# Performance work log

Hardware: AMD Instinct MI355X
Metric: run time of the kernel (lower is better)

The kernel has to match this reference:

```python
import jax, jax.numpy as jnp
import numpy as np

N = 50000      # nodes
E = 800000     # edges
G = 2000       # graphs
F_IN = 34
HID = 256
H = 8
D = 32         # HID // H
L = 5


def _layer_norm(x, g, b, eps=1e-5):
    m = x.mean(-1, keepdims=True)
    v = ((x - m) ** 2).mean(-1, keepdims=True)
    return (x - m) / jnp.sqrt(v + eps) * g + b


def _gelu(x):
    return jax.nn.gelu(x, approximate=False)  # torch exact GELU


def _segment_softmax(scores, seg, n):
    # scores: [E', H], seg: [E'] target node ids
    m = jax.ops.segment_max(scores, seg, num_segments=n)
    m = jnp.where(jnp.isfinite(m), m, 0.0)
    ex = jnp.exp(scores - m[seg])
    den = jax.ops.segment_sum(ex, seg, num_segments=n)
    return ex / (den[seg] + 1e-16)


def setup_inputs() -> dict:
    key = jax.random.key(0)
    ks = iter(jax.random.split(key, 64))

    def p(shape, fan):
        return (jax.random.normal(next(ks), shape, jnp.float32) / np.sqrt(fan)).astype(jnp.float32)

    inp = {}
    inp['x'] = jax.random.normal(next(ks), (N, F_IN), jnp.float32)
    inp['edge_index'] = jax.random.randint(next(ks), (2, E), 0, N, jnp.int32)
    inp['batch'] = jnp.sort(jax.random.randint(next(ks), (N,), 0, G, jnp.int32))

    # input embed
    inp['in_W'] = p((F_IN, HID), F_IN); inp['in_b'] = jnp.zeros((HID,), jnp.float32)
    inp['in_ln_g'] = jnp.ones((HID,), jnp.float32); inp['in_ln_b'] = jnp.zeros((HID,), jnp.float32)
    # 5 GATv2 layers (stacked on leading dim)
    inp['gat_Wl'] = p((L, HID, HID), HID); inp['gat_bl'] = jnp.zeros((L, HID), jnp.float32)
    inp['gat_Wr'] = p((L, HID, HID), HID); inp['gat_br'] = jnp.zeros((L, HID), jnp.float32)
    inp['gat_att'] = p((L, H, D), D)
    inp['gat_bias'] = jnp.zeros((L, HID), jnp.float32)
    inp['gat_ln_g'] = jnp.ones((L, HID), jnp.float32); inp['gat_ln_b'] = jnp.zeros((L, HID), jnp.float32)
    # TransformerConv
    inp['tr_Wq'] = p((HID, HID), HID); inp['tr_bq'] = jnp.zeros((HID,), jnp.float32)
    inp['tr_Wk'] = p((HID, HID), HID); inp['tr_bk'] = jnp.zeros((HID,), jnp.float32)
    inp['tr_Wv'] = p((HID, HID), HID); inp['tr_bv'] = jnp.zeros((HID,), jnp.float32)
    inp['tr_Wskip'] = p((HID, HID), HID); inp['tr_bskip'] = jnp.zeros((HID,), jnp.float32)
    inp['tr_ln_g'] = jnp.ones((HID,), jnp.float32); inp['tr_ln_b'] = jnp.zeros((HID,), jnp.float32)
    # output proj
    inp['out_W'] = p((2 * HID, 2 * HID), 2 * HID); inp['out_b'] = jnp.zeros((2 * HID,), jnp.float32)
    inp['out_ln_g'] = jnp.ones((2 * HID,), jnp.float32); inp['out_ln_b'] = jnp.zeros((2 * HID,), jnp.float32)
    return inp


def reference(x, edge_index, batch,
              in_W, in_b, in_ln_g, in_ln_b,
              gat_Wl, gat_bl, gat_Wr, gat_br, gat_att, gat_bias, gat_ln_g, gat_ln_b,
              tr_Wq, tr_bq, tr_Wk, tr_bk, tr_Wv, tr_bv, tr_Wskip, tr_bskip, tr_ln_g, tr_ln_b,
              out_W, out_b, out_ln_g, out_ln_b):
    # input embedding (dropout inactive in eval)
    h = _gelu(_layer_norm(x @ in_W + in_b, in_ln_g, in_ln_b))

    src, dst = edge_index[0], edge_index[1]  # PyG: row=source j, col=target i
    loops = jnp.arange(N, dtype=src.dtype)
    s2 = jnp.concatenate([src, loops])  # GATv2 adds self loops
    d2 = jnp.concatenate([dst, loops])

    for l in range(L):  # small fixed loop over layers
        xl = (h @ gat_Wl[l] + gat_bl[l]).reshape(N, H, D)  # source transform / message
        xr = (h @ gat_Wr[l] + gat_br[l]).reshape(N, H, D)  # target transform
        e = jax.nn.leaky_relu(xl[s2] + xr[d2], 0.2)        # [E', H, D]
        score = jnp.einsum('ehd,hd->eh', e, gat_att[l])
        alpha = _segment_softmax(score, d2, N)             # softmax over incoming edges
        out = jax.ops.segment_sum(xl[s2] * alpha[..., None], d2, num_segments=N)
        out = out.reshape(N, HID) + gat_bias[l]
        h = h + _gelu(_layer_norm(out, gat_ln_g[l], gat_ln_b[l]))

    # TransformerConv (no self loops, root_weight skip connection)
    q = (h @ tr_Wq + tr_bq).reshape(N, H, D)
    k = (h @ tr_Wk + tr_bk).reshape(N, H, D)
    v = (h @ tr_Wv + tr_bv).reshape(N, H, D)
    score = (q[dst] * k[src]).sum(-1) / jnp.sqrt(jnp.float32(D))  # [E, H]
    alpha = _segment_softmax(score, dst, N)
    out = jax.ops.segment_sum(v[src] * alpha[..., None], dst, num_segments=N).reshape(N, HID)
    out = out + h @ tr_Wskip + tr_bskip
    h = h + _layer_norm(out, tr_ln_g, tr_ln_b)

    # global mean + max pool
    cnt = jax.ops.segment_sum(jnp.ones((N,), h.dtype), batch, num_segments=G)
    h_mean = jax.ops.segment_sum(h, batch, num_segments=G) / jnp.maximum(cnt, 1.0)[:, None]
    h_max = jax.ops.segment_max(h, batch, num_segments=G)
    h_max = jnp.where(jnp.isfinite(h_max), h_max, 0.0)
    ge = jnp.concatenate([h_mean, h_max], axis=-1)  # [G, 512]
    return _gelu(_layer_norm(ge @ out_W + out_b, out_ln_g, out_ln_b))
```

## Files before the change

kernel.cpp:

```cpp
#include <hip/hip_runtime.h>
#include <math.h>

#define N_NODES 50000
#define N_EDGES 800000
#define N_GRAPH 2000
#define F_INPUT 34
#define HID 256
#define NLAYER 5

typedef __attribute__((ext_vector_type(8))) short short8;
typedef __attribute__((ext_vector_type(4))) float float4v;

__device__ __forceinline__ float gelu_f(float x) {
  return 0.5f * x * (1.0f + erff(x * 0.70710678118654752440f));
}
__device__ __forceinline__ unsigned short bfr(float f) {
  unsigned u = __float_as_uint(f);
  return (unsigned short)((u + 0x7fffu + ((u >> 16) & 1u)) >> 16);
}
__device__ __forceinline__ float b2f(unsigned short s) {
  return __uint_as_float(((unsigned)s) << 16);
}
__device__ __forceinline__ float4 ld4bf(const unsigned short* p) {
  ushort4 u = *(const ushort4*)p;
  float4 f;
  f.x = b2f(u.x); f.y = b2f(u.y); f.z = b2f(u.z); f.w = b2f(u.w);
  return f;
}
__device__ __forceinline__ void acp16(const unsigned short* g, unsigned short* l) {
  __builtin_amdgcn_global_load_lds(
      (const __attribute__((address_space(1))) void*)g,
      (__attribute__((address_space(3))) void*)l, 16, 0, 0);
}

__global__ __launch_bounds__(256) void gemm_bias(
    const float* __restrict__ A, const float* __restrict__ B,
    const float* __restrict__ bias, float* __restrict__ C,
    int M, int Nn, int K) {
  __shared__ float As[16][64];
  __shared__ float Bs[16][64];
  int tid = threadIdx.x;
  int tx = tid & 15, ty = tid >> 4;
  int row0 = blockIdx.y * 64;
  int col0 = blockIdx.x * 64;
  float acc[4][4] = {};
  int a_r = tid >> 2;
  int a_c = (tid & 3) * 4;
  int b_r = tid >> 4;
  int b_c = (tid & 15) * 4;

  for (int k0 = 0; k0 < K; k0 += 16) {
    int ar = row0 + a_r;
#pragma unroll
    for (int i = 0; i < 4; ++i) {
      int kc = k0 + a_c + i;
      As[a_c + i][a_r] = (ar < M && kc < K) ? A[(long)ar * K + kc] : 0.f;
    }
    int bk = k0 + b_r;
    if (bk < K) {
      float4 bv = *(const float4*)&B[(long)bk * Nn + col0 + b_c];
      Bs[b_r][b_c + 0] = bv.x; Bs[b_r][b_c + 1] = bv.y;
      Bs[b_r][b_c + 2] = bv.z; Bs[b_r][b_c + 3] = bv.w;
    } else {
      Bs[b_r][b_c + 0] = 0.f; Bs[b_r][b_c + 1] = 0.f;
      Bs[b_r][b_c + 2] = 0.f; Bs[b_r][b_c + 3] = 0.f;
    }
    __syncthreads();
#pragma unroll
    for (int kk = 0; kk < 16; ++kk) {
      float4 a = *(const float4*)&As[kk][ty * 4];
      float4 b = *(const float4*)&Bs[kk][tx * 4];
      float av[4] = {a.x, a.y, a.z, a.w};
      float bv[4] = {b.x, b.y, b.z, b.w};
#pragma unroll
      for (int i = 0; i < 4; ++i)
#pragma unroll
        for (int j = 0; j < 4; ++j) acc[i][j] += av[i] * bv[j];
    }
    __syncthreads();
  }
  float4 bi = *(const float4*)&bias[col0 + tx * 4];
  float bia[4] = {bi.x, bi.y, bi.z, bi.w};
#pragma unroll
  for (int i = 0; i < 4; ++i) {
    int r = row0 + ty * 4 + i;
    if (r < M) {
      float4 o;
      o.x = acc[i][0] + bia[0]; o.y = acc[i][1] + bia[1];
      o.z = acc[i][2] + bia[2]; o.w = acc[i][3] + bia[3];
      *(float4*)&C[(long)r * Nn + col0 + tx * 4] = o;
    }
  }
}

__global__ __launch_bounds__(256) void gemm_mfma(
    const unsigned short* __restrict__ A, const unsigned short* __restrict__ Bt,
    const float* __restrict__ bias, void* __restrict__ Cv,
    int M, int Nn, int K, int flags) {
  __shared__ unsigned short smem[12288];
  unsigned short* As = smem;
  unsigned short* Bs = smem + 4096;
  int tid = threadIdx.x;
  int wave = tid >> 6, lane = tid & 63;
  int row0 = blockIdx.y * 128;
  int col0 = blockIdx.x * 128;
  int wm0 = (wave >> 1) * 64;
  int wn0 = (wave & 1) * 64;
  int q = lane >> 4;
  int ln = lane & 15;

  int srow = wave * 16 + (lane >> 2);
  int scol = (lane & 3) * 8;
  int ra0 = min(row0 + srow, M - 1);
  int ra1 = min(row0 + srow + 64, M - 1);
  const unsigned short* pa0 = A + (size_t)ra0 * K + scol;
  const unsigned short* pa1 = A + (size_t)ra1 * K + scol;
  const unsigned short* pb0 = Bt + (size_t)(col0 + srow) * K + scol;
  const unsigned short* pb1 = Bt + (size_t)(col0 + srow + 64) * K + scol;
  unsigned short* la0 = As + wave * 512;
  unsigned short* la1 = As + wave * 512 + 2048;
  unsigned short* lb0 = Bs + wave * 512;
  unsigned short* lb1 = Bs + wave * 512 + 2048;

  float4v acc[4][4];
#pragma unroll
  for (int i = 0; i < 4; ++i)
#pragma unroll
    for (int j = 0; j < 4; ++j) acc[i][j] = (float4v)0.f;

  for (int k0 = 0; k0 < K; k0 += 32) {
    acp16(pa0 + k0, la0);
    acp16(pa1 + k0, la1);
    acp16(pb0 + k0, lb0);
    acp16(pb1 + k0, lb1);
    __syncthreads();
    short8 af[4], bf[4];
#pragma unroll
    for (int i = 0; i < 4; ++i)
      af[i] = *(const short8*)&As[(wm0 + i * 16 + ln) * 32 + q * 8];
#pragma unroll
    for (int j = 0; j < 4; ++j)
      bf[j] = *(const short8*)&Bs[(wn0 + j * 16 + ln) * 32 + q * 8];
#pragma unroll
    for (int i = 0; i < 4; ++i)
#pragma unroll
      for (int j = 0; j < 4; ++j)
        acc[i][j] = __builtin_amdgcn_mfma_f32_16x16x32_bf16(af[i], bf[j], acc[i][j], 0, 0, 0);
    __syncthreads();
  }
  int rb = (lane >> 4) * 4;
  if (flags & 2) {
    unsigned short* Cb = (unsigned short*)Cv;
    unsigned short* eb = smem + wave * 2560;
#pragma unroll
    for (int p = 0; p < 2; ++p) {
#pragma unroll
      for (int jj = 0; jj < 2; ++jj) {
        int j = p * 2 + jj;
        float bv = bias[col0 + wn0 + j * 16 + ln];
#pragma unroll
        for (int i = 0; i < 4; ++i)
#pragma unroll
          for (int r = 0; r < 4; ++r)
            eb[(i * 16 + rb + r) * 40 + jj * 16 + ln] = bfr(acc[i][j][r] + bv);
      }
      int grow = row0 + wm0 + lane;
      uint4 w0 = *(uint4*)&eb[lane * 40 + 0];
      uint4 w1 = *(uint4*)&eb[lane * 40 + 8];
      uint4 w2 = *(uint4*)&eb[lane * 40 + 16];
      uint4 w3 = *(uint4*)&eb[lane * 40 + 24];
      if (grow < M) {
        unsigned short* dst = Cb + (size_t)grow * Nn + col0 + wn0 + p * 32;
        *(uint4*)&dst[0] = w0;
        *(uint4*)&dst[8] = w1;
        *(uint4*)&dst[16] = w2;
        *(uint4*)&dst[24] = w3;
      }
    }
  } else {
    float* C = (float*)Cv;
#pragma unroll
    for (int j = 0; j < 4; ++j) {
      int col = col0 + wn0 + j * 16 + ln;
      float bv = bias[col];
#pragma unroll
      for (int i = 0; i < 4; ++i)
#pragma unroll
        for (int r = 0; r < 4; ++r) {
          int row = row0 + wm0 + i * 16 + rb + r;
          if (row < M) C[(size_t)row * Nn + col] = acc[i][j][r] + bv;
        }
    }
  }
}

__global__ __launch_bounds__(256) void prep_w(
    const float* __restrict__ Wl, const float* __restrict__ Wr,
    const float* __restrict__ Wq, const float* __restrict__ Wk,
    const float* __restrict__ Wv, const float* __restrict__ Wsk,
    unsigned short* __restrict__ out) {
  __shared__ float t[32][33];
  int m = blockIdx.z;
  const float* W = (m < 10) ? (((m & 1) ? Wr : Wl) + (size_t)(m >> 1) * 65536)
                 : (m == 10) ? Wq : (m == 11) ? Wk : (m == 12) ? Wv : Wsk;
  int k0 = blockIdx.y * 32, n0 = blockIdx.x * 32;
  int r = threadIdx.x >> 5, c = threadIdx.x & 31;
  for (int rr = r; rr < 32; rr += 8)
    t[rr][c] = W[(size_t)(k0 + rr) * HID + n0 + c];
  __syncthreads();
  unsigned short* o = out + (size_t)m * 65536;
  for (int rr = r; rr < 32; rr += 8)
    o[(size_t)(n0 + rr) * HID + k0 + c] = bfr(t[c][rr]);
}

__global__ __launch_bounds__(256) void prep_wout(const float* __restrict__ W,
                                                 unsigned short* __restrict__ o) {
  __shared__ float t[32][33];
  int k0 = blockIdx.y * 32, n0 = blockIdx.x * 32;
  int r = threadIdx.x >> 5, c = threadIdx.x & 31;
  for (int rr = r; rr < 32; rr += 8)
    t[rr][c] = W[(size_t)(k0 + rr) * 512 + n0 + c];
  __syncthreads();
  for (int rr = r; rr < 32; rr += 8)
    o[(size_t)(n0 + rr) * 512 + k0 + c] = bfr(t[c][rr]);
}

__global__ __launch_bounds__(256) void prep_bias(
    const float* __restrict__ bl, const float* __restrict__ br,
    const float* __restrict__ bq, const float* __restrict__ bk,
    const float* __restrict__ bv, float* __restrict__ out) {
  int i = blockIdx.x * 256 + threadIdx.x;
  if (i < 2560) {
    int l = i >> 9, c = i & 511;
    out[i] = (c < 256) ? bl[l * 256 + c] : br[l * 256 + (c - 256)];
  } else if (i < 3328) {
    int j = i - 2560;
    out[i] = (j < 256) ? bq[j] : (j < 512) ? bk[j - 256] : bv[j - 512];
  }
}

__global__ __launch_bounds__(256) void ln_act(
    const float* __restrict__ in, const float* __restrict__ gam,
    const float* __restrict__ bet, float* __restrict__ out,
    unsigned short* __restrict__ outb,
    int n_rows, int width, int do_gelu) {
  int wid = blockIdx.x * 4 + (threadIdx.x >> 6);
  int lane = threadIdx.x & 63;
  if (wid >= n_rows) return;
  int chunks = width >> 8;
  float4 v[2];
  float s = 0.f;
  for (int c = 0; c < chunks; ++c) {
    int off = c * 256 + lane * 4;
    float4 t = *(const float4*)&in[(size_t)wid * width + off];
    v[c] = t;
    s += t.x + t.y + t.z + t.w;
  }
  for (int o = 1; o < 64; o <<= 1) s += __shfl_xor(s, o);
  float mean = s / (float)width;
  float vs = 0.f;
  for (int c = 0; c < chunks; ++c) {
    float dx = v[c].x - mean, dy = v[c].y - mean, dz = v[c].z - mean, dw = v[c].w - mean;
    vs += dx * dx + dy * dy + dz * dz + dw * dw;
  }
  for (int o = 1; o < 64; o <<= 1) vs += __shfl_xor(vs, o);
  float inv = rsqrtf(vs / (float)width + 1e-5f);
  for (int c = 0; c < chunks; ++c) {
    int off = c * 256 + lane * 4;
    float4 g4 = *(const float4*)&gam[off];
    float4 b4 = *(const float4*)&bet[off];
    float y[4] = {(v[c].x - mean) * inv * g4.x + b4.x,
                  (v[c].y - mean) * inv * g4.y + b4.y,
                  (v[c].z - mean) * inv * g4.z + b4.z,
                  (v[c].w - mean) * inv * g4.w + b4.w};
    if (do_gelu) {
#pragma unroll
      for (int i = 0; i < 4; ++i) y[i] = gelu_f(y[i]);
    }
    size_t idx = (size_t)wid * width + off;
    float4 o4 = {y[0], y[1], y[2], y[3]};
    *(float4*)&out[idx] = o4;
    if (outb) {
      ushort4 ob = {bfr(y[0]), bfr(y[1]), bfr(y[2]), bfr(y[3])};
      *(ushort4*)&outb[idx] = ob;
    }
  }
}

__global__ __launch_bounds__(256) void edge_count(const int* __restrict__ ei,
                                                  int* __restrict__ counts) {
  int e = blockIdx.x * 256 + threadIdx.x;
  if (e < N_EDGES) atomicAdd(&counts[ei[N_EDGES + e]], 1);
}

__global__ __launch_bounds__(1024) void scan1(const int* __restrict__ counts,
                                              int* __restrict__ indptr,
                                              int* __restrict__ bsums, int n) {
  __shared__ int sm[1024];
  int tid = threadIdx.x;
  int i = blockIdx.x * 1024 + tid;
  int v = (i < n) ? counts[i] : 0;
  sm[tid] = v;
  __syncthreads();
  for (int off = 1; off < 1024; off <<= 1) {
    int t = (tid >= off) ? sm[tid - off] : 0;
    __syncthreads();
    sm[tid] += t;
    __syncthreads();
  }
  if (i < n) indptr[i] = sm[tid] - v;
  if (tid == 1023) bsums[blockIdx.x] = sm[1023];
}

__global__ void scan2(int* __restrict__ bsums, int nb) {
  if (threadIdx.x == 0 && blockIdx.x == 0) {
    int acc = 0;
    for (int i = 0; i < nb; ++i) { int t = bsums[i]; bsums[i] = acc; acc += t; }
  }
}

__global__ __launch_bounds__(256) void scan3(const int* __restrict__ bsums,
                                             int* __restrict__ indptr,
                                             int* __restrict__ cursor, int n) {
  int i = blockIdx.x * 256 + threadIdx.x;
  if (i < n) {
    int v = indptr[i] + bsums[i >> 10];
    indptr[i] = v;
    cursor[i] = v;
  }
  if (i == 0) indptr[n] = N_EDGES;
}

__global__ __launch_bounds__(256) void edge_scatter(const int* __restrict__ ei,
                                                    int* __restrict__ cursor,
                                                    int* __restrict__ esrc) {
  int e = blockIdx.x * 256 + threadIdx.x;
  if (e < N_EDGES) {
    int d = ei[N_EDGES + e];
    int p = atomicAdd(&cursor[d], 1);
    esrc[p] = ei[e];
  }
}

#define GAT_EDGE(f)                                                        \
  {                                                                        \
    float ex = f.x + xri.x; ex = ex > 0.f ? ex : 0.2f * ex;                \
    float ey = f.y + xri.y; ey = ey > 0.f ? ey : 0.2f * ey;                \
    float ez = f.z + xri.z; ez = ez > 0.f ? ez : 0.2f * ez;                \
    float ew = f.w + xri.w; ew = ew > 0.f ? ew : 0.2f * ew;                \
    float p = ex * a4.x + ey * a4.y + ez * a4.z + ew * a4.w;               \
    p += __shfl_xor(p, 1); p += __shfl_xor(p, 2); p += __shfl_xor(p, 4);   \
    float wgt = __expf(fminf(p - m0, 60.f));                               \
    ax += wgt * f.x; ay += wgt * f.y; az += wgt * f.z; aw += wgt * f.w;    \
    lsum += wgt;                                                           \
  }

__global__ __launch_bounds__(256) void gat_agg(
    const unsigned short* __restrict__ xlr, const float* __restrict__ att,
    const int* __restrict__ indptr, const int* __restrict__ esrc,
    const float* __restrict__ pre_bias, const float* __restrict__ gam,
    const float* __restrict__ bet, float* __restrict__ h,
    unsigned short* __restrict__ hb) {
  int wid = blockIdx.x * 4 + (threadIdx.x >> 6);
  int lane = threadIdx.x & 63;
  if (wid >= N_NODES) return;
  float4 xri = ld4bf(&xlr[(size_t)wid * 512 + 256 + lane * 4]);
  float4 a4 = *(const float4*)&att[lane * 4];
  int beg = indptr[wid], end = indptr[wid + 1];

  float m0, lsum, ax, ay, az, aw;
  {
    float4 f = ld4bf(&xlr[(size_t)wid * 512 + lane * 4]);
    float ex = f.x + xri.x; ex = ex > 0.f ? ex : 0.2f * ex;
    float ey = f.y + xri.y; ey = ey > 0.f ? ey : 0.2f * ey;
    float ez = f.z + xri.z; ez = ez > 0.f ? ez : 0.2f * ez;
    float ew = f.w + xri.w; ew = ew > 0.f ? ew : 0.2f * ew;
    float p = ex * a4.x + ey * a4.y + ez * a4.z + ew * a4.w;
    p += __shfl_xor(p, 1); p += __shfl_xor(p, 2); p += __shfl_xor(p, 4);
    m0 = p; lsum = 1.f;
    ax = f.x; ay = f.y; az = f.z; aw = f.w;
  }
  int e = beg;
  for (; e + 3 < end; e += 4) {
    int j0 = esrc[e], j1 = esrc[e + 1], j2 = esrc[e + 2], j3 = esrc[e + 3];
    float4 f0 = ld4bf(&xlr[(size_t)j0 * 512 + lane * 4]);
    float4 f1 = ld4bf(&xlr[(size_t)j1 * 512 + lane * 4]);
    float4 f2 = ld4bf(&xlr[(size_t)j2 * 512 + lane * 4]);
    float4 f3 = ld4bf(&xlr[(size_t)j3 * 512 + lane * 4]);
    GAT_EDGE(f0); GAT_EDGE(f1); GAT_EDGE(f2); GAT_EDGE(f3);
  }
  for (; e < end; ++e) {
    int j = esrc[e];
    float4 f = ld4bf(&xlr[(size_t)j * 512 + lane * 4]);
    GAT_EDGE(f);
  }
  float inv = 1.f / (lsum + 1e-16f);
  float4 pb = *(const float4*)&pre_bias[lane * 4];
  float y0 = ax * inv + pb.x, y1 = ay * inv + pb.y;
  float y2 = az * inv + pb.z, y3 = aw * inv + pb.w;
  float s = y0 + y1 + y2 + y3;
  for (int o = 1; o < 64; o <<= 1) s += __shfl_xor(s, o);
  float mean = s * (1.f / 256.f);
  float d0 = y0 - mean, d1 = y1 - mean, d2 = y2 - mean, d3 = y3 - mean;
  float vs = d0 * d0 + d1 * d1 + d2 * d2 + d3 * d3;
  for (int o = 1; o < 64; o <<= 1) vs += __shfl_xor(vs, o);
  float inv2 = rsqrtf(vs * (1.f / 256.f) + 1e-5f);
  float4 g4 = *(const float4*)&gam[lane * 4];
  float4 b4 = *(const float4*)&bet[lane * 4];
  y0 = gelu_f(d0 * inv2 * g4.x + b4.x);
  y1 = gelu_f(d1 * inv2 * g4.y + b4.y);
  y2 = gelu_f(d2 * inv2 * g4.z + b4.z);
  y3 = gelu_f(d3 * inv2 * g4.w + b4.w);
  size_t idx = (size_t)wid * HID + lane * 4;
  float4 r4 = *(const float4*)&h[idx];
  y0 += r4.x; y1 += r4.y; y2 += r4.z; y3 += r4.w;
  float4 o4 = {y0, y1, y2, y3};
  *(float4*)&h[idx] = o4;
  ushort4 ob = {bfr(y0), bfr(y1), bfr(y2), bfr(y3)};
  *(ushort4*)&hb[idx] = ob;
}

#define TR_EDGE(kj, vj)                                                    \
  {                                                                        \
    float p = qi.x * kj.x + qi.y * kj.y + qi.z * kj.z + qi.w * kj.w;       \
    p += __shfl_xor(p, 1); p += __shfl_xor(p, 2); p += __shfl_xor(p, 4);   \
    float wgt = __expf(fminf(p * scale, 60.f));                            \
    ax += wgt * vj.x; ay += wgt * vj.y; az += wgt * vj.z; aw += wgt * vj.w;\
    lsum += wgt;                                                           \
  }

__global__ __launch_bounds__(256) void tr_agg(
    const unsigned short* __restrict__ qkv, const int* __restrict__ indptr,
    const int* __restrict__ esrc, const unsigned short* __restrict__ skipb,
    const float* __restrict__ gam, const float* __restrict__ bet,
    float* __restrict__ h) {
  int wid = blockIdx.x * 4 + (threadIdx.x >> 6);
  int lane = threadIdx.x & 63;
  if (wid >= N_NODES) return;
  float4 qi = ld4bf(&qkv[(size_t)wid * 768 + lane * 4]);
  int beg = indptr[wid], end = indptr[wid + 1];
  float lsum = 0.f;
  float ax = 0.f, ay = 0.f, az = 0.f, aw = 0.f;
  const float scale = 0.17677669529663687f;
  int e = beg;
  for (; e + 1 < end; e += 2) {
    int j0 = esrc[e], j1 = esrc[e + 1];
    float4 k0 = ld4bf(&qkv[(size_t)j0 * 768 + 256 + lane * 4]);
    float4 v0 = ld4bf(&qkv[(size_t)j0 * 768 + 512 + lane * 4]);
    float4 k1 = ld4bf(&qkv[(size_t)j1 * 768 + 256 + lane * 4]);
    float4 v1 = ld4bf(&qkv[(size_t)j1 * 768 + 512 + lane * 4]);
    TR_EDGE(k0, v0); TR_EDGE(k1, v1);
  }
  if (e < end) {
    int j = esrc[e];
    float4 kj = ld4bf(&qkv[(size_t)j * 768 + 256 + lane * 4]);
    float4 vj = ld4bf(&qkv[(size_t)j * 768 + 512 + lane * 4]);
    TR_EDGE(kj, vj);
  }
  float inv = 1.f / (lsum + 1e-16f);
  size_t idx = (size_t)wid * HID + lane * 4;
  float4 sk = ld4bf(&skipb[idx]);
  float y0 = ax * inv + sk.x, y1 = ay * inv + sk.y;
  float y2 = az * inv + sk.z, y3 = aw * inv + sk.w;
  float s = y0 + y1 + y2 + y3;
  for (int o = 1; o < 64; o <<= 1) s += __shfl_xor(s, o);
  float mean = s * (1.f / 256.f);
  float d0 = y0 - mean, d1 = y1 - mean, d2 = y2 - mean, d3 = y3 - mean;
  float vs = d0 * d0 + d1 * d1 + d2 * d2 + d3 * d3;
  for (int o = 1; o < 64; o <<= 1) vs += __shfl_xor(vs, o);
  float inv2 = rsqrtf(vs * (1.f / 256.f) + 1e-5f);
  float4 g4 = *(const float4*)&gam[lane * 4];
  float4 b4 = *(const float4*)&bet[lane * 4];
  float4 r4 = *(const float4*)&h[idx];
  float4 o4;
  o4.x = r4.x + d0 * inv2 * g4.x + b4.x;
  o4.y = r4.y + d1 * inv2 * g4.y + b4.y;
  o4.z = r4.z + d2 * inv2 * g4.z + b4.z;
  o4.w = r4.w + d3 * inv2 * g4.w + b4.w;
  *(float4*)&h[idx] = o4;
}

__global__ __launch_bounds__(256) void graph_bounds(const int* __restrict__ batch,
                                                    int* __restrict__ gptr) {
  int i = blockIdx.x * 256 + threadIdx.x;
  if (i >= N_NODES) return;
  int b0 = batch[i];
  if (i == 0)
    for (int g = 0; g <= b0; ++g) gptr[g] = 0;
  int b1 = (i + 1 < N_NODES) ? batch[i + 1] : N_GRAPH;
  for (int g = b0 + 1; g <= b1; ++g) gptr[g] = i + 1;
}

__global__ __launch_bounds__(256) void pool_seg(
    const float* __restrict__ h, const int* __restrict__ gptr,
    unsigned short* __restrict__ geb) {
  int g = blockIdx.x, c = threadIdx.x;
  int s = gptr[g], e = gptr[g + 1];
  float sum = 0.f, mx = -INFINITY;
  for (int r = s; r < e; ++r) {
    float vv = h[(size_t)r * HID + c];
    sum += vv;
    mx = fmaxf(mx, vv);
  }
  int cnt = e - s;
  geb[(size_t)g * 512 + c] = bfr(sum / (float)max(cnt, 1));
  geb[(size_t)g * 512 + 256 + c] = bfr(cnt ? mx : 0.f);
}

static inline void mfma_launch(const unsigned short* A, const unsigned short* Bt,
                               const float* bias, void* C, int M, int Nn, int K,
                               int flags, hipStream_t s) {
  dim3 grid(Nn / 128, (M + 127) / 128);
  gemm_mfma<<<grid, 256, 0, s>>>(A, Bt, bias, C, M, Nn, K, flags);
}

extern "C" void kernel_launch(void* const* d_in, const int* in_sizes, int n_in,
                              void* d_out, int out_size, void* d_ws, size_t ws_size,
                              hipStream_t stream) {
  const float* x       = (const float*)d_in[0];
  const int*   ei      = (const int*)d_in[1];
  const int*   batch   = (const int*)d_in[2];
  const float* in_W    = (const float*)d_in[3];
  const float* in_b    = (const float*)d_in[4];
  const float* in_ln_g = (const float*)d_in[5];
  const float* in_ln_b = (const float*)d_in[6];
  const float* gat_Wl  = (const float*)d_in[7];
  const float* gat_bl  = (const float*)d_in[8];
  const float* gat_Wr  = (const float*)d_in[9];
  const float* gat_br  = (const float*)d_in[10];
  const float* gat_att = (const float*)d_in[11];
  const float* gat_bias= (const float*)d_in[12];
  const float* gat_ln_g= (const float*)d_in[13];
  const float* gat_ln_b= (const float*)d_in[14];
  const float* tr_Wq   = (const float*)d_in[15];
  const float* tr_bq   = (const float*)d_in[16];
  const float* tr_Wk   = (const float*)d_in[17];
  const float* tr_bk   = (const float*)d_in[18];
  const float* tr_Wv   = (const float*)d_in[19];
  const float* tr_bv   = (const float*)d_in[20];
  const float* tr_Wsk  = (const float*)d_in[21];
  const float* tr_bsk  = (const float*)d_in[22];
  const float* tr_ln_g = (const float*)d_in[23];
  const float* tr_ln_b = (const float*)d_in[24];
  const float* out_W   = (const float*)d_in[25];
  const float* out_b   = (const float*)d_in[26];
  const float* out_ln_g= (const float*)d_in[27];
  const float* out_ln_b= (const float*)d_in[28];

  char* w = (char*)d_ws;
  auto take = [&](size_t bytes) -> char* {
    char* p = w;
    w += (bytes + 255) & ~(size_t)255;
    return p;
  };
  const size_t NB = (size_t)N_NODES * HID * sizeof(float);
  float* h    = (float*)take(NB);
  float* aggO = (float*)take(NB);
  unsigned short* hb  = (unsigned short*)take((size_t)N_NODES * HID * 2);
  unsigned short* xq  = (unsigned short*)take((size_t)N_NODES * 768 * 2);
  unsigned short* wbuf= (unsigned short*)take((size_t)(14 * 65536 + 262144) * 2);
  float* bcat = (float*)take(3328 * sizeof(float));
  int* indptr = (int*)take((N_NODES + 1) * sizeof(int));
  int* cursor = (int*)take(N_NODES * sizeof(int));
  int* counts = (int*)take(N_NODES * sizeof(int));
  int* esrc   = (int*)take(N_EDGES * sizeof(int));
  int* bsums  = (int*)take(64 * sizeof(int));
  unsigned short* skipb = (unsigned short*)aggO;
  char* w2 = (char*)xq;
  auto take2 = [&](size_t bytes) -> char* {
    char* p = w2;
    w2 += (bytes + 255) & ~(size_t)255;
    return p;
  };
  int* gptr = (int*)take2((N_GRAPH + 1) * sizeof(int));
  unsigned short* geb = (unsigned short*)take2((size_t)N_GRAPH * 512 * 2);
  float* tbuf = (float*)take2((size_t)N_GRAPH * 512 * sizeof(float));

  const int EB = (N_EDGES + 255) / 256;
  const int WB = (N_NODES + 3) / 4;
  const int NSB = (N_NODES + 1023) / 1024;

  {
    dim3 g(8, 8, 14);
    prep_w<<<g, 256, 0, stream>>>(gat_Wl, gat_Wr, tr_Wq, tr_Wk, tr_Wv, tr_Wsk, wbuf);
    dim3 g2(16, 16);
    prep_wout<<<g2, 256, 0, stream>>>(out_W, wbuf + (size_t)14 * 65536);
    prep_bias<<<13, 256, 0, stream>>>(gat_bl, gat_br, tr_bq, tr_bk, tr_bv, bcat);
  }

  hipMemsetAsync(counts, 0, N_NODES * sizeof(int), stream);
  edge_count<<<EB, 256, 0, stream>>>(ei, counts);
  scan1<<<NSB, 1024, 0, stream>>>(counts, indptr, bsums, N_NODES);
  scan2<<<1, 64, 0, stream>>>(bsums, NSB);
  scan3<<<(N_NODES + 255) / 256, 256, 0, stream>>>(bsums, indptr, cursor, N_NODES);
  edge_scatter<<<EB, 256, 0, stream>>>(ei, cursor, esrc);

  {
    dim3 grid(HID / 64, (N_NODES + 63) / 64);
    gemm_bias<<<grid, 256, 0, stream>>>(x, in_W, in_b, aggO, N_NODES, HID, F_INPUT);
  }
  ln_act<<<WB, 256, 0, stream>>>(aggO, in_ln_g, in_ln_b, h, hb, N_NODES, HID, 1);

  for (int l = 0; l < NLAYER; ++l) {
    mfma_launch(hb, wbuf + (size_t)(2 * l) * 65536, bcat + l * 512, xq,
                N_NODES, 512, HID, 2, stream);
    gat_agg<<<WB, 256, 0, stream>>>(xq, gat_att + l * HID, indptr, esrc,
                                    gat_bias + l * HID, gat_ln_g + l * HID,
                                    gat_ln_b + l * HID, h, hb);
  }

  mfma_launch(hb, wbuf + (size_t)13 * 65536, tr_bsk, skipb,
              N_NODES, HID, HID, 2, stream);
  mfma_launch(hb, wbuf + (size_t)10 * 65536, bcat + 2560, xq,
              N_NODES, 768, HID, 2, stream);
  tr_agg<<<WB, 256, 0, stream>>>(xq, indptr, esrc, skipb, tr_ln_g, tr_ln_b, h);

  graph_bounds<<<(N_NODES + 255) / 256, 256, 0, stream>>>(batch, gptr);
  pool_seg<<<N_GRAPH, 256, 0, stream>>>(h, gptr, geb);

  mfma_launch(geb, wbuf + (size_t)14 * 65536, out_b, tbuf,
              N_GRAPH, 512, 512, 0, stream);
  ln_act<<<(N_GRAPH + 3) / 4, 256, 0, stream>>>(tbuf, out_ln_g, out_ln_b,
                                                (float*)d_out, nullptr,
                                                N_GRAPH, 512, 1);
}
```

Before: 1.169 ms.

## Split each node's edge aggregation across two waves and combine via LDS

The GAT and Transformer aggregation kernels now give each destination node two wavefronts instead of one. Each wave handles alternating edges, and the partial sums and softmax denominators are combined through shared memory. The aim is to double memory-level parallelism on the latency-bound gather, at the cost of a block barrier, extra LDS traffic and twice as many blocks. Both waves recompute the self term and the final LayerNorm runs on one wave only; the per-node bounds check is dropped because N is even.

```diff
diff --git a/kernel.cpp b/kernel.cpp
--- a/kernel.cpp
+++ b/kernel.cpp
@@ -361,9 +361,11 @@
     const float* __restrict__ pre_bias, const float* __restrict__ gam,
     const float* __restrict__ bet, float* __restrict__ h,
     unsigned short* __restrict__ hb) {
-  int wid = blockIdx.x * 4 + (threadIdx.x >> 6);
-  int lane = threadIdx.x & 63;
-  if (wid >= N_NODES) return;
+  __shared__ float comb[2][5][64];
+  int tid = threadIdx.x;
+  int wave = tid >> 6, lane = tid & 63;
+  int pair = wave >> 1, half = wave & 1;
+  int wid = blockIdx.x * 2 + pair;
   float4 xri = ld4bf(&xlr[(size_t)wid * 512 + 256 + lane * 4]);
   float4 a4 = *(const float4*)&att[lane * 4];
   int beg = indptr[wid], end = indptr[wid + 1];
@@ -377,23 +379,38 @@
     float ew = f.w + xri.w; ew = ew > 0.f ? ew : 0.2f * ew;
     float p = ex * a4.x + ey * a4.y + ez * a4.z + ew * a4.w;
     p += __shfl_xor(p, 1); p += __shfl_xor(p, 2); p += __shfl_xor(p, 4);
-    m0 = p; lsum = 1.f;
-    ax = f.x; ay = f.y; az = f.z; aw = f.w;
-  }
-  int e = beg;
-  for (; e + 3 < end; e += 4) {
-    int j0 = esrc[e], j1 = esrc[e + 1], j2 = esrc[e + 2], j3 = esrc[e + 3];
+    m0 = p;
+    if (half == 0) {
+      lsum = 1.f; ax = f.x; ay = f.y; az = f.z; aw = f.w;
+    } else {
+      lsum = 0.f; ax = 0.f; ay = 0.f; az = 0.f; aw = 0.f;
+    }
+  }
+  int e = beg + half;
+  for (; e + 6 < end; e += 8) {
+    int j0 = esrc[e], j1 = esrc[e + 2], j2 = esrc[e + 4], j3 = esrc[e + 6];
     float4 f0 = ld4bf(&xlr[(size_t)j0 * 512 + lane * 4]);
     float4 f1 = ld4bf(&xlr[(size_t)j1 * 512 + lane * 4]);
     float4 f2 = ld4bf(&xlr[(size_t)j2 * 512 + lane * 4]);
     float4 f3 = ld4bf(&xlr[(size_t)j3 * 512 + lane * 4]);
     GAT_EDGE(f0); GAT_EDGE(f1); GAT_EDGE(f2); GAT_EDGE(f3);
   }
-  for (; e < end; ++e) {
+  for (; e < end; e += 2) {
     int j = esrc[e];
     float4 f = ld4bf(&xlr[(size_t)j * 512 + lane * 4]);
     GAT_EDGE(f);
   }
+  if (half) {
+    comb[pair][0][lane] = ax; comb[pair][1][lane] = ay;
+    comb[pair][2][lane] = az; comb[pair][3][lane] = aw;
+    comb[pair][4][lane] = lsum;
+  }
+  __syncthreads();
+  if (half) return;
+  ax += comb[pair][0][lane]; ay += comb[pair][1][lane];
+  az += comb[pair][2][lane]; aw += comb[pair][3][lane];
+  lsum += comb[pair][4][lane];
+
   float inv = 1.f / (lsum + 1e-16f);
   float4 pb = *(const float4*)&pre_bias[lane * 4];
   float y0 = ax * inv + pb.x, y1 = ay * inv + pb.y;
@@ -407,13 +424,12 @@
   float inv2 = rsqrtf(vs * (1.f / 256.f) + 1e-5f);
   float4 g4 = *(const float4*)&gam[lane * 4];
   float4 b4 = *(const float4*)&bet[lane * 4];
-  y0 = gelu_f(d0 * inv2 * g4.x + b4.x);
-  y1 = gelu_f(d1 * inv2 * g4.y + b4.y);
-  y2 = gelu_f(d2 * inv2 * g4.z + b4.z);
-  y3 = gelu_f(d3 * inv2 * g4.w + b4.w);
   size_t idx = (size_t)wid * HID + lane * 4;
   float4 r4 = *(const float4*)&h[idx];
-  y0 += r4.x; y1 += r4.y; y2 += r4.z; y3 += r4.w;
+  y0 = gelu_f(d0 * inv2 * g4.x + b4.x) + r4.x;
+  y1 = gelu_f(d1 * inv2 * g4.y + b4.y) + r4.y;
+  y2 = gelu_f(d2 * inv2 * g4.z + b4.z) + r4.z;
+  y3 = gelu_f(d3 * inv2 * g4.w + b4.w) + r4.w;
   float4 o4 = {y0, y1, y2, y3};
   *(float4*)&h[idx] = o4;
   ushort4 ob = {bfr(y0), bfr(y1), bfr(y2), bfr(y3)};
@@ -434,29 +450,42 @@
     const int* __restrict__ esrc, const unsigned short* __restrict__ skipb,
     const float* __restrict__ gam, const float* __restrict__ bet,
     float* __restrict__ h) {
-  int wid = blockIdx.x * 4 + (threadIdx.x >> 6);
-  int lane = threadIdx.x & 63;
-  if (wid >= N_NODES) return;
+  __shared__ float comb[2][5][64];
+  int tid = threadIdx.x;
+  int wave = tid >> 6, lane = tid & 63;
+  int pair = wave >> 1, half = wave & 1;
+  int wid = blockIdx.x * 2 + pair;
   float4 qi = ld4bf(&qkv[(size_t)wid * 768 + lane * 4]);
   int beg = indptr[wid], end = indptr[wid + 1];
   float lsum = 0.f;
   float ax = 0.f, ay = 0.f, az = 0.f, aw = 0.f;
   const float scale = 0.17677669529663687f;
-  int e = beg;
-  for (; e + 1 < end; e += 2) {
-    int j0 = esrc[e], j1 = esrc[e + 1];
+  int e = beg + half;
+  for (; e + 2 < end; e += 4) {
+    int j0 = esrc[e], j1 = esrc[e + 2];
     float4 k0 = ld4bf(&qkv[(size_t)j0 * 768 + 256 + lane * 4]);
     float4 v0 = ld4bf(&qkv[(size_t)j0 * 768 + 512 + lane * 4]);
     float4 k1 = ld4bf(&qkv[(size_t)j1 * 768 + 256 + lane * 4]);
     float4 v1 = ld4bf(&qkv[(size_t)j1 * 768 + 512 + lane * 4]);
     TR_EDGE(k0, v0); TR_EDGE(k1, v1);
   }
-  if (e < end) {
+  for (; e < end; e += 2) {
     int j = esrc[e];
     float4 kj = ld4bf(&qkv[(size_t)j * 768 + 256 + lane * 4]);
     float4 vj = ld4bf(&qkv[(size_t)j * 768 + 512 + lane * 4]);
     TR_EDGE(kj, vj);
   }
+  if (half) {
+    comb[pair][0][lane] = ax; comb[pair][1][lane] = ay;
+    comb[pair][2][lane] = az; comb[pair][3][lane] = aw;
+    comb[pair][4][lane] = lsum;
+  }
+  __syncthreads();
+  if (half) return;
+  ax += comb[pair][0][lane]; ay += comb[pair][1][lane];
+  az += comb[pair][2][lane]; aw += comb[pair][3][lane];
+  lsum += comb[pair][4][lane];
+
   float inv = 1.f / (lsum + 1e-16f);
   size_t idx = (size_t)wid * HID + lane * 4;
   float4 sk = ld4bf(&skipb[idx]);
@@ -578,6 +607,7 @@
 
   const int EB = (N_EDGES + 255) / 256;
   const int WB = (N_NODES + 3) / 4;
+  const int WB2 = N_NODES / 2;
   const int NSB = (N_NODES + 1023) / 1024;
 
   {
@@ -604,16 +634,16 @@
   for (int l = 0; l < NLAYER; ++l) {
     mfma_launch(hb, wbuf + (size_t)(2 * l) * 65536, bcat + l * 512, xq,
                 N_NODES, 512, HID, 2, stream);
-    gat_agg<<<WB, 256, 0, stream>>>(xq, gat_att + l * HID, indptr, esrc,
-                                    gat_bias + l * HID, gat_ln_g + l * HID,
-                                    gat_ln_b + l * HID, h, hb);
+    gat_agg<<<WB2, 256, 0, stream>>>(xq, gat_att + l * HID, indptr, esrc,
+                                     gat_bias + l * HID, gat_ln_g + l * HID,
+                                     gat_ln_b + l * HID, h, hb);
   }
 
   mfma_launch(hb, wbuf + (size_t)13 * 65536, tr_bsk, skipb,
               N_NODES, HID, HID, 2, stream);
   mfma_launch(hb, wbuf + (size_t)10 * 65536, bcat + 2560, xq,
               N_NODES, 768, HID, 2, stream);
-  tr_agg<<<WB, 256, 0, stream>>>(xq, indptr, esrc, skipb, tr_ln_g, tr_ln_b, h);
+  tr_agg<<<WB2, 256, 0, stream>>>(xq, indptr, esrc, skipb, tr_ln_g, tr_ln_b, h);
 
   graph_bounds<<<(N_NODES + 255) / 256, 256, 0, stream>>>(batch, gptr);
   pool_seg<<<N_GRAPH, 256, 0, stream>>>(h, gptr, geb);
```

Result: slower. 1.205 ms (+3.1%).
